# Kernel optimization log

Hardware: AMD Instinct MI355X
Metric: run time of the kernel (lower is better)

The kernel has to match this reference:

```python
import jax, jax.numpy as jnp
import numpy as np

N1, N2 = 30, 60
T, B = 1024, 2048
LIMIT = 1.0 / np.sqrt(N1 + N2)


def setup_inputs() -> dict:
    key = jax.random.key(0)
    ks = jax.random.split(key, 9)
    u = lambda k, shape: jax.random.uniform(k, shape, jnp.float32, -LIMIT, LIMIT)
    inp = jax.random.normal(ks[0], (T, B, 1), jnp.float32)
    # noise is randn*0.1 per step in the original; pre-sampled here for determinism
    noise1 = jax.random.normal(ks[1], (T, B, N1), jnp.float32) * 0.1
    noise2 = jax.random.normal(ks[2], (T, B, N2), jnp.float32) * 0.1
    W11 = u(ks[3], (N1, N1))
    W22 = u(ks[4], (N2, N2))
    W21 = u(ks[5], (N2, N1))
    W21_mask = (jax.random.uniform(ks[6], (N2, N1)) < 0.3).astype(jnp.float32)
    Win = u(ks[7], (N1, 1))
    Wout = u(ks[8], (1, N2))
    return {"inp": inp, "noise1": noise1, "noise2": noise2, "W11": W11,
            "W22": W22, "W21": W21, "W21_mask": W21_mask, "Win": Win, "Wout": Wout}


def reference(inp, noise1, noise2, W11, W22, W21, W21_mask, Win, Wout):
    # masked feedforward weight, computed once
    W21m = W21 * W21_mask  # (N2, N1)
    Bsz = inp.shape[1]
    r1_0 = jnp.zeros((Bsz, N1), inp.dtype)
    r2_0 = jnp.zeros((Bsz, N2), inp.dtype)

    def step(carry, xs):
        r1, r2 = carry
        x_t, n1, n2 = xs  # (B,1), (B,N1), (B,N2)
        r1_out = jnp.tanh(r1 @ W11.T + x_t @ Win.T + n1)          # (B, N1)
        r2_out = jnp.tanh(r2 @ W22.T + r1_out @ W21m.T + n2)      # (B, N2)
        y = r2_out @ Wout.T                                        # (B, 1)
        return (r1_out, r2_out), y

    _, ys = jax.lax.scan(step, (r1_0, r2_0), (inp, noise1, noise2))
    return ys  # (T, B, 1)
```

## Files before the change

kernel.cpp:

```cpp
#include <hip/hip_runtime.h>

#define N1 30
#define N2 60
#define T_STEPS 1024
#define BATCH 2048

__device__ __forceinline__ float lane_bcast(float v, int l) {
  return __int_as_float(__builtin_amdgcn_readlane(__float_as_int(v), l));
}

__device__ __forceinline__ float fast_tanh(float x) {
  float e = __expf(2.0f * x);
  float r = __builtin_amdgcn_rcpf(e + 1.0f);
  return fmaf(-2.0f, r, 1.0f);
}

__global__ __launch_bounds__(256, 2) void hrnn_kernel(
    const float* __restrict__ inp,
    const float* __restrict__ noise1,
    const float* __restrict__ noise2,
    const float* __restrict__ W11,
    const float* __restrict__ W22,
    const float* __restrict__ W21,
    const float* __restrict__ W21m,
    const float* __restrict__ Win,
    const float* __restrict__ Wout,
    float* __restrict__ out)
{
  const int lane = threadIdx.x & 63;
  int b = blockIdx.x * 4 + (threadIdx.x >> 6);
  b = __builtin_amdgcn_readfirstlane(b);

  const int i1 = (lane < N1) ? lane : 0;
  const int i2 = (lane < N2) ? lane : 0;

  float w11[N1], w21[N1], w22[N2];
#pragma unroll
  for (int j = 0; j < N1; ++j) w11[j] = W11[i1 * N1 + j];
#pragma unroll
  for (int j = 0; j < N1; ++j) w21[j] = W21[i2 * N1 + j] * W21m[i2 * N1 + j];
#pragma unroll
  for (int j = 0; j < N2; ++j) w22[j] = W22[i2 * N2 + j];
  const float win  = (lane < N1) ? Win[lane]  : 0.0f;
  const float wout = (lane < N2) ? Wout[lane] : 0.0f;

  float s1 = 0.0f, s2 = 0.0f;

  unsigned n1i = (unsigned)b * N1 + (unsigned)i1;
  unsigned n2i = (unsigned)b * N2 + (unsigned)i2;
  unsigned xi  = (unsigned)b;
  unsigned yi  = (unsigned)b;

  float x_c  = inp[xi];
  float n1_c = noise1[n1i];
  float n2_c = noise2[n2i];

  for (int t = 0; t < T_STEPS; ++t) {
    const unsigned adv = (t < T_STEPS - 1) ? 1u : 0u;
    xi  += BATCH * adv;
    n1i += (unsigned)(BATCH * N1) * adv;
    n2i += (unsigned)(BATCH * N2) * adv;
    const float x_n  = inp[xi];
    const float n1_n = noise1[n1i];
    const float n2_n = noise2[n2i];

    float a0 = fmaf(win, x_c, n1_c);
    float a1 = 0.0f;
#pragma unroll
    for (int j = 0; j < N1; j += 2) {
      a0 = fmaf(w11[j],     lane_bcast(s1, j),     a0);
      a1 = fmaf(w11[j + 1], lane_bcast(s1, j + 1), a1);
    }
    const float s1n = fast_tanh(a0 + a1);

    float c0 = n2_c, c1 = 0.0f, c2 = 0.0f, c3 = 0.0f;
#pragma unroll
    for (int j = 0; j < N2; j += 4) {
      c0 = fmaf(w22[j],     lane_bcast(s2, j),     c0);
      c1 = fmaf(w22[j + 1], lane_bcast(s2, j + 1), c1);
      c2 = fmaf(w22[j + 2], lane_bcast(s2, j + 2), c2);
      c3 = fmaf(w22[j + 3], lane_bcast(s2, j + 3), c3);
    }
#pragma unroll
    for (int j = 0; j < N1; j += 2) {
      c0 = fmaf(w21[j],     lane_bcast(s1n, j),     c0);
      c1 = fmaf(w21[j + 1], lane_bcast(s1n, j + 1), c1);
    }
    const float s2n = fast_tanh((c0 + c1) + (c2 + c3));

    float p = wout * s2n;
#pragma unroll
    for (int off = 32; off; off >>= 1) p += __shfl_xor(p, off, 64);
    if (lane == 0) out[yi] = p;
    yi += BATCH;

    s1 = s1n; s2 = s2n;
    x_c = x_n; n1_c = n1_n; n2_c = n2_n;
  }
}

extern "C" void kernel_launch(void* const* d_in, const int* in_sizes, int n_in,
                              void* d_out, int out_size, void* d_ws, size_t ws_size,
                              hipStream_t stream) {
  const float* inp    = (const float*)d_in[0];
  const float* noise1 = (const float*)d_in[1];
  const float* noise2 = (const float*)d_in[2];
  const float* W11    = (const float*)d_in[3];
  const float* W22    = (const float*)d_in[4];
  const float* W21    = (const float*)d_in[5];
  const float* W21m   = (const float*)d_in[6];
  const float* Win    = (const float*)d_in[7];
  const float* Wout   = (const float*)d_in[8];
  float* out = (float*)d_out;

  dim3 grid(BATCH / 4);
  dim3 block(256);
  hipLaunchKernelGGL(hrnn_kernel, grid, block, 0, stream,
                     inp, noise1, noise2, W11, W22, W21, W21m, Win, Wout, out);
}
```

Baseline: 1.712 ms.

## Pack weights and hidden states as fp16 pairs and use dot2 accumulation

Stores the recurrent weights and broadcast hidden states as packed half2 values and replaces pairs of FMAs and readlanes with one fdot2 per pair plus one readlane. This halves the readlane and FMA count on the serial per-step critical path and halves weight register usage. In exchange it adds a shuffle and a pack per layer each step, and the fp16 quantisation of states and weights may compound error over 1024 recurrent steps.

```diff
diff --git a/kernel.cpp b/kernel.cpp
--- a/kernel.cpp
+++ b/kernel.cpp
@@ -5,14 +5,34 @@
 #define T_STEPS 1024
 #define BATCH 2048
 
-__device__ __forceinline__ float lane_bcast(float v, int l) {
-  return __int_as_float(__builtin_amdgcn_readlane(__float_as_int(v), l));
-}
+typedef _Float16 h2_t __attribute__((ext_vector_type(2)));
 
 __device__ __forceinline__ float fast_tanh(float x) {
   float e = __expf(2.0f * x);
   float r = __builtin_amdgcn_rcpf(e + 1.0f);
   return fmaf(-2.0f, r, 1.0f);
+}
+
+__device__ __forceinline__ float dot2(unsigned a, unsigned b, float acc) {
+#if __has_builtin(__builtin_amdgcn_fdot2)
+  return __builtin_amdgcn_fdot2(__builtin_bit_cast(h2_t, a),
+                                __builtin_bit_cast(h2_t, b), acc, false);
+#else
+  h2_t ha = __builtin_bit_cast(h2_t, a);
+  h2_t hb = __builtin_bit_cast(h2_t, b);
+  return fmaf((float)ha.x, (float)hb.x, fmaf((float)ha.y, (float)hb.y, acc));
+#endif
+}
+
+__device__ __forceinline__ unsigned pack_f16(float lo, float hi) {
+  h2_t p;
+  p.x = (_Float16)lo;
+  p.y = (_Float16)hi;
+  return __builtin_bit_cast(unsigned, p);
+}
+
+__device__ __forceinline__ unsigned lane_bcast_u(unsigned v, int l) {
+  return (unsigned)__builtin_amdgcn_readlane((int)v, l);
 }
 
 __global__ __launch_bounds__(256, 2) void hrnn_kernel(
@@ -34,17 +54,21 @@
   const int i1 = (lane < N1) ? lane : 0;
   const int i2 = (lane < N2) ? lane : 0;
 
-  float w11[N1], w21[N1], w22[N2];
+  unsigned w11p[N1 / 2], w21p[N1 / 2], w22p[N2 / 2];
 #pragma unroll
-  for (int j = 0; j < N1; ++j) w11[j] = W11[i1 * N1 + j];
+  for (int m = 0; m < N1 / 2; ++m)
+    w11p[m] = pack_f16(W11[i1 * N1 + 2 * m], W11[i1 * N1 + 2 * m + 1]);
 #pragma unroll
-  for (int j = 0; j < N1; ++j) w21[j] = W21[i2 * N1 + j] * W21m[i2 * N1 + j];
+  for (int m = 0; m < N1 / 2; ++m)
+    w21p[m] = pack_f16(W21[i2 * N1 + 2 * m] * W21m[i2 * N1 + 2 * m],
+                       W21[i2 * N1 + 2 * m + 1] * W21m[i2 * N1 + 2 * m + 1]);
 #pragma unroll
-  for (int j = 0; j < N2; ++j) w22[j] = W22[i2 * N2 + j];
+  for (int m = 0; m < N2 / 2; ++m)
+    w22p[m] = pack_f16(W22[i2 * N2 + 2 * m], W22[i2 * N2 + 2 * m + 1]);
   const float win  = (lane < N1) ? Win[lane]  : 0.0f;
   const float wout = (lane < N2) ? Wout[lane] : 0.0f;
 
-  float s1 = 0.0f, s2 = 0.0f;
+  unsigned s1pk = 0u, s2pk = 0u;
 
   unsigned n1i = (unsigned)b * N1 + (unsigned)i1;
   unsigned n2i = (unsigned)b * N2 + (unsigned)i2;
@@ -64,37 +88,41 @@
     const float n1_n = noise1[n1i];
     const float n2_n = noise2[n2i];
 
-    float a0 = fmaf(win, x_c, n1_c);
-    float a1 = 0.0f;
+    float a[2];
+    a[0] = fmaf(win, x_c, n1_c);
+    a[1] = 0.0f;
 #pragma unroll
-    for (int j = 0; j < N1; j += 2) {
-      a0 = fmaf(w11[j],     lane_bcast(s1, j),     a0);
-      a1 = fmaf(w11[j + 1], lane_bcast(s1, j + 1), a1);
+    for (int m = 0; m < N1 / 2; ++m) {
+      const unsigned p = lane_bcast_u(s1pk, 2 * m);
+      a[m & 1] = dot2(w11p[m], p, a[m & 1]);
     }
-    const float s1n = fast_tanh(a0 + a1);
+    const float s1n = fast_tanh(a[0] + a[1]);
+    const float s1o = __shfl_xor(s1n, 1, 64);
+    const unsigned s1npk = pack_f16(s1n, s1o);
 
-    float c0 = n2_c, c1 = 0.0f, c2 = 0.0f, c3 = 0.0f;
+    float c[4];
+    c[0] = n2_c; c[1] = 0.0f; c[2] = 0.0f; c[3] = 0.0f;
 #pragma unroll
-    for (int j = 0; j < N2; j += 4) {
-      c0 = fmaf(w22[j],     lane_bcast(s2, j),     c0);
-      c1 = fmaf(w22[j + 1], lane_bcast(s2, j + 1), c1);
-      c2 = fmaf(w22[j + 2], lane_bcast(s2, j + 2), c2);
-      c3 = fmaf(w22[j + 3], lane_bcast(s2, j + 3), c3);
+    for (int m = 0; m < N2 / 2; ++m) {
+      const unsigned p = lane_bcast_u(s2pk, 2 * m);
+      c[m & 3] = dot2(w22p[m], p, c[m & 3]);
     }
 #pragma unroll
-    for (int j = 0; j < N1; j += 2) {
-      c0 = fmaf(w21[j],     lane_bcast(s1n, j),     c0);
-      c1 = fmaf(w21[j + 1], lane_bcast(s1n, j + 1), c1);
+    for (int m = 0; m < N1 / 2; ++m) {
+      const unsigned p = lane_bcast_u(s1npk, 2 * m);
+      c[m & 3] = dot2(w21p[m], p, c[m & 3]);
     }
-    const float s2n = fast_tanh((c0 + c1) + (c2 + c3));
+    const float s2n = fast_tanh((c[0] + c[1]) + (c[2] + c[3]));
+    const float s2o = __shfl_xor(s2n, 1, 64);
+    const unsigned s2npk = pack_f16(s2n, s2o);
 
-    float p = wout * s2n;
+    float p3 = wout * s2n;
 #pragma unroll
-    for (int off = 32; off; off >>= 1) p += __shfl_xor(p, off, 64);
-    if (lane == 0) out[yi] = p;
+    for (int off = 32; off; off >>= 1) p3 += __shfl_xor(p3, off, 64);
+    if (lane == 0) out[yi] = p3;
     yi += BATCH;
 
-    s1 = s1n; s2 = s2n;
+    s1pk = s1npk; s2pk = s2npk;
     x_c = x_n; n1_c = n1_n; n2_c = n2_n;
   }
 }
```

New measurement: 1.747 ms. 1.02x slower.
